# Kernel tuning notes

Measured on AMD Instinct MI355X. Metric: run time of the kernel, lower is better.

## Reference

```python
import jax, jax.numpy as jnp
import numpy as np

B, S, D, H, FF = 2, 2048, 1024, 16, 4096
DK = D // H
LOCAL_WINDOW, STRIDE = 128, 128
NEG = -1000000000.0
EPS = 1e-5


def _layernorm(x, g, b):
    mu = jnp.mean(x, axis=-1, keepdims=True)
    var = jnp.mean(jnp.square(x - mu), axis=-1, keepdims=True)
    return (x - mu) * jax.lax.rsqrt(var + EPS) * g + b


def _strided_mask(seq):
    # allowed(i, j): j <= i and (i-j <= local_window or (i-j) % stride == 0)
    i = jnp.arange(seq)[:, None]
    j = jnp.arange(seq)[None, :]
    d = i - j
    return (d >= 0) & ((d <= LOCAL_WINDOW) | (d % STRIDE == 0))  # [S, S] bool


def setup_inputs() -> dict:
    key = jax.random.key(0)
    ks = jax.random.split(key, 18)
    w = lambda k, shape: jax.random.normal(k, shape, jnp.float32) * 0.02
    return {
        "x": jax.random.normal(ks[0], (B, S, D), jnp.float32),
        "mask": jnp.ones((1, 1, S, S), jnp.int32),
        "Wq": w(ks[1], (D, D)), "bq": jnp.zeros((D,), jnp.float32),
        "Wk": w(ks[2], (D, D)), "bk": jnp.zeros((D,), jnp.float32),
        "Wv": w(ks[3], (D, D)), "bv": jnp.zeros((D,), jnp.float32),
        "Wo": w(ks[4], (D, D)), "bo": jnp.zeros((D,), jnp.float32),
        "W1": w(ks[5], (D, FF)), "bf1": jnp.zeros((FF,), jnp.float32),
        "W2": w(ks[6], (FF, D)), "bf2": jnp.zeros((D,), jnp.float32),
        "g1": jnp.ones((D,), jnp.float32), "bl1": jnp.zeros((D,), jnp.float32),
        "g2": jnp.ones((D,), jnp.float32), "bl2": jnp.zeros((D,), jnp.float32),
    }


def reference(x, mask, Wq, bq, Wk, bk, Wv, bv, Wo, bo,
              W1, bf1, W2, bf2, g1, bl1, g2, bl2):
    b, s, d = x.shape
    sm = _strided_mask(s)[None, None]  # [1,1,S,S]

    # pre-LN self-attention
    n = _layernorm(x, g1, bl1)
    split = lambda t: t.reshape(b, s, H, DK).transpose(0, 2, 1, 3)  # [B,H,S,DK]
    q = split(n @ Wq + bq)
    k = split(n @ Wk + bk)
    v = split(n @ Wv + bv)

    scores = jnp.einsum('bhqd,bhkd->bhqk', q, k) / jnp.sqrt(jnp.float32(DK))
    scores = jnp.where(sm, scores, NEG)          # strided/local mask
    scores = jnp.where(mask == 0, NEG, scores)   # user mask
    attn = jax.nn.softmax(scores, axis=-1)
    o = jnp.einsum('bhqk,bhkd->bhqd', attn, v)
    o = o.transpose(0, 2, 1, 3).reshape(b, s, d) @ Wo + bo
    x = x + o

    # pre-LN FFN (GELU exact, matching torch nn.GELU default)
    n2 = _layernorm(x, g2, bl2)
    ff = jax.nn.gelu(n2 @ W1 + bf1, approximate=False) @ W2 + bf2
    return x + ff
```

## Files before the change

kernel.cpp:

```cpp
#include <hip/hip_runtime.h>
#include <math.h>

typedef unsigned int u32;
typedef unsigned short u16;

#define B_  2
#define S_  2048
#define D_  1024
#define H_  16
#define DK_ 64
#define FF_ 4096
#define NEG_ -1000000000.0f

typedef __attribute__((ext_vector_type(8))) short short8;
typedef __attribute__((ext_vector_type(4))) float floatx4;
typedef __attribute__((ext_vector_type(4))) unsigned short ushort4_t;

__device__ inline u16 f2b(float f) {
    union { float f; u32 u; } v; v.f = f;
    u32 r = (v.u + 0x7fffu + ((v.u >> 16) & 1u)) >> 16;
    return (u16)r;
}
__device__ inline float b2f(u16 b) {
    union { u32 u; float f; } v; v.u = ((u32)b) << 16;
    return v.f;
}

__device__ inline void gl_lds16(const u16* g, u16* l) {
    __builtin_amdgcn_global_load_lds((const __attribute__((address_space(1))) u32*)g,
                                     (__attribute__((address_space(3))) u32*)l, 16, 0, 0);
}

__global__ void tconv4(const float* __restrict__ W0, const float* __restrict__ W1_,
                       const float* __restrict__ W2_, const float* __restrict__ W3,
                       u16* __restrict__ dstBase) {
    __shared__ float tile[32][33];
    int z = blockIdx.z;
    const float* Wm = (z == 0) ? W0 : (z == 1) ? W1_ : (z == 2) ? W2_ : W3;
    u16* Wt = dstBase + (size_t)z * 1024 * 1024;
    const int K = 1024, N = 1024;
    int n0 = blockIdx.x * 32, k0 = blockIdx.y * 32;
    int tx = threadIdx.x & 31, ty = threadIdx.x >> 5;
#pragma unroll
    for (int r = 0; r < 32; r += 8)
        tile[ty + r][tx] = Wm[(size_t)(k0 + ty + r) * N + n0 + tx];
    __syncthreads();
#pragma unroll
    for (int r = 0; r < 32; r += 8)
        Wt[(size_t)(n0 + ty + r) * K + k0 + tx] = f2b(tile[tx][ty + r]);
}

__global__ void tconv(const float* __restrict__ Wm, u16* __restrict__ Wt, int K, int N) {
    __shared__ float tile[32][33];
    int n0 = blockIdx.x * 32, k0 = blockIdx.y * 32;
    int tx = threadIdx.x & 31, ty = threadIdx.x >> 5;
#pragma unroll
    for (int r = 0; r < 32; r += 8)
        tile[ty + r][tx] = Wm[(size_t)(k0 + ty + r) * N + n0 + tx];
    __syncthreads();
#pragma unroll
    for (int r = 0; r < 32; r += 8)
        Wt[(size_t)(n0 + ty + r) * K + k0 + tx] = f2b(tile[tx][ty + r]);
}

__global__ void catbias(const float* __restrict__ bq, const float* __restrict__ bk,
                        const float* __restrict__ bv, float* __restrict__ out) {
    int i = blockIdx.x * 256 + threadIdx.x;
    float v = (i < 1024) ? bq[i] : (i < 2048) ? bk[i - 1024] : bv[i - 2048];
    out[i] = v;
}

__global__ void ln_bf16(const float* __restrict__ x, const float* __restrict__ g,
                        const float* __restrict__ b, u16* __restrict__ out) {
    int row = blockIdx.x;
    int t = threadIdx.x;
    const float* xr = x + (size_t)row * D_;
    __shared__ float red[256];

    float s = 0.f;
    for (int i = t; i < D_; i += 256) s += xr[i];
    red[t] = s; __syncthreads();
    for (int off = 128; off > 0; off >>= 1) {
        if (t < off) red[t] += red[t + off];
        __syncthreads();
    }
    float mu = red[0] * (1.0f / D_);
    __syncthreads();

    float vs = 0.f;
    for (int i = t; i < D_; i += 256) { float d = xr[i] - mu; vs += d * d; }
    red[t] = vs; __syncthreads();
    for (int off = 128; off > 0; off >>= 1) {
        if (t < off) red[t] += red[t + off];
        __syncthreads();
    }
    float rstd = rsqrtf(red[0] * (1.0f / D_) + 1e-5f);

    u16* outr = out + (size_t)row * D_;
    for (int i = t; i < D_; i += 256)
        outr[i] = f2b((xr[i] - mu) * rstd * g[i] + b[i]);
}

template <int EPI>
__global__ __launch_bounds__(256)
void gemm_bt(const u16* __restrict__ A, const u16* __restrict__ Bt,
             const float* __restrict__ bias, const float* __restrict__ R,
             void* __restrict__ Cv, int M, int N, int K, int ldA, int ldB) {
    __shared__ u16 As[2 * 128 * 32];
    __shared__ u16 Bs[2 * 128 * 32];
    int tid = threadIdx.x;
    int lane = tid & 63, w = tid >> 6;
    int wm = w >> 1, wn = w & 1;
    int m0 = blockIdx.x * 128, n0 = blockIdx.y * 128;
    size_t koff = (size_t)blockIdx.z * K;

    floatx4 acc[4][4];
#pragma unroll
    for (int a = 0; a < 4; a++)
#pragma unroll
        for (int b2 = 0; b2 < 4; b2++) acc[a][b2] = (floatx4){0.f, 0.f, 0.f, 0.f};

    int r4 = lane >> 2;
    int qg = ((lane & 3) ^ ((lane >> 3) & 3)) * 8;
    const u16* Ag0 = A + (size_t)(m0 + w * 16 + r4) * ldA + koff + qg;
    const u16* Bg0 = Bt + (size_t)(n0 + w * 16 + r4) * ldB + koff + qg;
    u16* Al = As + (w * 16) * 32;
    u16* Bl = Bs + (w * 16) * 32;

    int c = lane & 15, g = lane >> 4;
    int sw = (g ^ ((c >> 1) & 3)) * 8;
    const u16* pa[4];
    const u16* pb[4];
#pragma unroll
    for (int a = 0; a < 4; a++) pa[a] = &As[(wm * 64 + a * 16 + c) * 32 + sw];
#pragma unroll
    for (int b2 = 0; b2 < 4; b2++) pb[b2] = &Bs[(wn * 64 + b2 * 16 + c) * 32 + sw];

    for (int k0 = 0; k0 < K; k0 += 64) {
        __syncthreads();
        gl_lds16(Ag0 + k0,                      Al);
        gl_lds16(Ag0 + k0 + (size_t)64 * ldA,   Al + 64 * 32);
        gl_lds16(Ag0 + k0 + 32,                 Al + 128 * 32);
        gl_lds16(Ag0 + k0 + 32 + (size_t)64 * ldA, Al + 192 * 32);
        gl_lds16(Bg0 + k0,                      Bl);
        gl_lds16(Bg0 + k0 + (size_t)64 * ldB,   Bl + 64 * 32);
        gl_lds16(Bg0 + k0 + 32,                 Bl + 128 * 32);
        gl_lds16(Bg0 + k0 + 32 + (size_t)64 * ldB, Bl + 192 * 32);
        __syncthreads();

        short8 fa[4], fb[4];
#pragma unroll
        for (int a = 0; a < 4; a++) fa[a] = *(const short8*)pa[a];
#pragma unroll
        for (int b2 = 0; b2 < 4; b2++) fb[b2] = *(const short8*)pb[b2];
#pragma unroll
        for (int a = 0; a < 4; a++)
#pragma unroll
            for (int b2 = 0; b2 < 4; b2++)
                acc[a][b2] = __builtin_amdgcn_mfma_f32_16x16x32_bf16(fa[a], fb[b2], acc[a][b2], 0, 0, 0);
#pragma unroll
        for (int a = 0; a < 4; a++) fa[a] = *(const short8*)(pa[a] + 128 * 32);
#pragma unroll
        for (int b2 = 0; b2 < 4; b2++) fb[b2] = *(const short8*)(pb[b2] + 128 * 32);
#pragma unroll
        for (int a = 0; a < 4; a++)
#pragma unroll
            for (int b2 = 0; b2 < 4; b2++)
                acc[a][b2] = __builtin_amdgcn_mfma_f32_16x16x32_bf16(fa[a], fb[b2], acc[a][b2], 0, 0, 0);
    }

    int mb = m0 + wm * 64, nb = n0 + wn * 64;
#pragma unroll
    for (int a = 0; a < 4; a++) {
#pragma unroll
        for (int b2 = 0; b2 < 4; b2++) {
            int mrow = mb + a * 16 + (lane >> 4) * 4;
            int ncol = nb + b2 * 16 + (lane & 15);
            float bv = (EPI == 3) ? 0.f : bias[ncol];
#pragma unroll
            for (int r = 0; r < 4; r++) {
                int m = mrow + r;
                float vvv = acc[a][b2][r] + bv;
                if (EPI == 0) {
                    int which = ncol >> 10, col = ncol & 1023;
                    int bb = m >> 11, ss = m & 2047, hh = col >> 6, dk = col & 63;
                    ((u16*)Cv)[(size_t)which * ((size_t)B_ * S_ * D_) +
                               ((((size_t)bb * H_ + hh) * S_) + ss) * DK_ + dk] = f2b(vvv);
                } else if (EPI == 1) {
                    ((float*)Cv)[(size_t)m * N + ncol] = vvv + R[(size_t)m * N + ncol];
                } else if (EPI == 2) {
                    ((u16*)Cv)[(size_t)m * N + ncol] =
                        f2b(0.5f * vvv * (1.f + erff(vvv * 0.70710678118654752f)));
                } else {
                    ((u16*)Cv)[(size_t)blockIdx.z * M * N + (size_t)m * N + ncol] = f2b(vvv);
                }
            }
        }
    }
}

__global__ __launch_bounds__(256)
void ffn2_merge(const u16* __restrict__ P, const float* __restrict__ x1,
                const float* __restrict__ bf2, float* __restrict__ out) {
    const size_t MN = (size_t)B_ * S_ * D_;
    int e = (blockIdx.x * 256 + threadIdx.x) * 4;
    float4 xv = *(const float4*)&x1[e];
    float4 bv = *(const float4*)&bf2[e & 1023];
    float o0 = xv.x + bv.x, o1 = xv.y + bv.y, o2 = xv.z + bv.z, o3 = xv.w + bv.w;
#pragma unroll
    for (int z = 0; z < 4; z++) {
        ushort4_t pv = *(const ushort4_t*)&P[z * MN + e];
        o0 += b2f(pv[0]); o1 += b2f(pv[1]); o2 += b2f(pv[2]); o3 += b2f(pv[3]);
    }
    *(float4*)&out[e] = (float4){o0, o1, o2, o3};
}

__global__ __launch_bounds__(256)
void attn3(const u16* __restrict__ q, const u16* __restrict__ k,
           const u16* __restrict__ v, const int* __restrict__ mask,
           u16* __restrict__ ob) {
    __shared__ u16 Qs[64 * 72];
    __shared__ u16 Kw[192 * 72];
    __shared__ u16 Vt[64 * 200];
    __shared__ u16 Vband[4][16 * 64];
    __shared__ float sb[64][17];

    const int i0 = blockIdx.x * 64;
    const int bh = blockIdx.y;
    const int b  = bh >> 4, h = bh & 15;
    const int t  = threadIdx.x;
    const int lane = t & 63, w = t >> 6;
    const int c = lane & 15, g = lane >> 4;
    const int qloc16 = w * 16;

    const u16* qg = q + ((size_t)bh * S_ + i0) * DK_;
    const u16* kg = k + (size_t)bh * S_ * DK_;
    const u16* vg = v + (size_t)bh * S_ * DK_;

    const int wlo = (i0 >= 128) ? i0 - 128 : 0;
    const int wn  = i0 + 64 - wlo;
    const int nb  = (i0 >= 256) ? (i0 >> 7) - 1 : 0;
    const int jb0 = i0 & 127;
    const int dd0 = i0 - wlo;

    for (int e = t; e < 64 * 8; e += 256) {
        int row = e >> 3, dc = e & 7;
        *(short8*)&Qs[row * 72 + dc * 8] = *(const short8*)(qg + row * 64 + dc * 8);
    }
    for (int e = t; e < wn * 8; e += 256) {
        int row = e >> 3, dc = e & 7;
        *(short8*)&Kw[row * 72 + dc * 8] = *(const short8*)(kg + (size_t)(wlo + row) * 64 + dc * 8);
    }
#pragma unroll
    for (int dc = 0; dc < 8; dc++) {
        for (int jl = t; jl < 192; jl += 256) {
            short8 val = {0, 0, 0, 0, 0, 0, 0, 0};
            if (jl < wn) val = *(const short8*)(vg + (size_t)(wlo + jl) * 64 + dc * 8);
#pragma unroll
            for (int i = 0; i < 8; i++) Vt[(dc * 8 + i) * 200 + jl] = (u16)val[i];
        }
    }
    __syncthreads();

    for (int m = 0; m < nb; m++) {
        int jb = jb0 + (m << 7);
        int jrow = jb + qloc16 + c;
        float p = 0.f;
#pragma unroll
        for (int kc = 0; kc < 2; kc++) {
            short8 kv = *(const short8*)(kg + (size_t)jrow * 64 + kc * 32 + g * 8);
            short8 qv = *(const short8*)&Qs[(qloc16 + c) * 72 + kc * 32 + g * 8];
#pragma unroll
            for (int i = 0; i < 8; i++) p += b2f((u16)qv[i]) * b2f((u16)kv[i]);
        }
        p += __shfl_xor(p, 16);
        p += __shfl_xor(p, 32);
        if (g == 0) {
            int qi = i0 + qloc16 + c;
            float s = p * 0.125f;
            if (mask[(size_t)qi * S_ + jrow] == 0) s = NEG_;
            sb[qloc16 + c][m] = s;
        }
    }

    floatx4 sc[12];
#pragma unroll
    for (int ct = 0; ct < 12; ct++) sc[ct] = (floatx4){0.f, 0.f, 0.f, 0.f};
    short8 fa0 = *(const short8*)&Qs[(qloc16 + c) * 72 + g * 8];
    short8 fa1 = *(const short8*)&Qs[(qloc16 + c) * 72 + 32 + g * 8];
#pragma unroll
    for (int ct = 0; ct < 12; ct++) {
        short8 fb0 = *(const short8*)&Kw[(ct * 16 + c) * 72 + g * 8];
        short8 fb1 = *(const short8*)&Kw[(ct * 16 + c) * 72 + 32 + g * 8];
        sc[ct] = __builtin_amdgcn_mfma_f32_16x16x32_bf16(fa0, fb0, sc[ct], 0, 0, 0);
        sc[ct] = __builtin_amdgcn_mfma_f32_16x16x32_bf16(fa1, fb1, sc[ct], 0, 0, 0);
    }

#pragma unroll
    for (int ct = 0; ct < 12; ct++) {
        int cidx = ct * 16 + c;
        int j = wlo + cidx;
#pragma unroll
        for (int r = 0; r < 4; r++) {
            int qloc = qloc16 + g * 4 + r;
            int d = dd0 + qloc - cidx;
            float s = sc[ct][r] * 0.125f;
            bool ok = false;
            if (d >= 0 && d <= 128) ok = (mask[(size_t)(i0 + qloc) * S_ + j] != 0);
            sc[ct][r] = ok ? s : NEG_;
        }
    }

    float mv[4], inv[4];
#pragma unroll
    for (int r = 0; r < 4; r++) {
        float mm = -1e30f;
#pragma unroll
        for (int ct = 0; ct < 12; ct++) mm = fmaxf(mm, sc[ct][r]);
        mm = fmaxf(mm, __shfl_xor(mm, 1));
        mm = fmaxf(mm, __shfl_xor(mm, 2));
        mm = fmaxf(mm, __shfl_xor(mm, 4));
        mm = fmaxf(mm, __shfl_xor(mm, 8));
        int qloc = qloc16 + g * 4 + r;
        for (int m = 0; m < nb; m++) mm = fmaxf(mm, sb[qloc][m]);
        float sum = 0.f;
#pragma unroll
        for (int ct = 0; ct < 12; ct++) {
            float e = __expf(sc[ct][r] - mm);
            sc[ct][r] = e;
            sum += e;
        }
        sum += __shfl_xor(sum, 1);
        sum += __shfl_xor(sum, 2);
        sum += __shfl_xor(sum, 4);
        sum += __shfl_xor(sum, 8);
        for (int m = 0; m < nb; m++) sum += __expf(sb[qloc][m] - mm);
        mv[r] = mm;
        inv[r] = 1.f / sum;
    }

    __syncthreads();
    u16* P = Kw;
#pragma unroll
    for (int ct = 0; ct < 12; ct++) {
#pragma unroll
        for (int r = 0; r < 4; r++) {
            int qloc = qloc16 + g * 4 + r;
            P[qloc * 200 + ct * 16 + c] = f2b(sc[ct][r]);
        }
    }

    floatx4 o[4];
#pragma unroll
    for (int nt = 0; nt < 4; nt++) o[nt] = (floatx4){0.f, 0.f, 0.f, 0.f};
#pragma unroll
    for (int ks = 0; ks < 6; ks++) {
        short8 pa = *(const short8*)&P[(qloc16 + c) * 200 + ks * 32 + g * 8];
#pragma unroll
        for (int nt = 0; nt < 4; nt++) {
            short8 vb = *(const short8*)&Vt[(nt * 16 + c) * 200 + ks * 32 + g * 8];
            o[nt] = __builtin_amdgcn_mfma_f32_16x16x32_bf16(pa, vb, o[nt], 0, 0, 0);
        }
    }

    for (int m = 0; m < nb; m++) {
        int jb = jb0 + (m << 7);
        asm volatile("s_waitcnt lgkmcnt(0)" ::: "memory");
        __builtin_amdgcn_wave_barrier();
        gl_lds16(vg + (size_t)(jb + qloc16 + (lane >> 3)) * 64 + (lane & 7) * 8, &Vband[w][0]);
        gl_lds16(vg + (size_t)(jb + qloc16 + 8 + (lane >> 3)) * 64 + (lane & 7) * 8, &Vband[w][512]);
        asm volatile("s_waitcnt vmcnt(0)" ::: "memory");
        __builtin_amdgcn_wave_barrier();
#pragma unroll
        for (int r = 0; r < 4; r++) {
            int qloc = qloc16 + g * 4 + r;
            float pb = __expf(sb[qloc][m] - mv[r]);
#pragma unroll
            for (int nt = 0; nt < 4; nt++)
                o[nt][r] += pb * b2f(Vband[w][(g * 4 + r) * 64 + nt * 16 + c]);
        }
    }

#pragma unroll
    for (int nt = 0; nt < 4; nt++) {
#pragma unroll
        for (int r = 0; r < 4; r++) {
            int qi = i0 + qloc16 + g * 4 + r;
            ob[((size_t)b * S_ + qi) * D_ + h * 64 + nt * 16 + c] = f2b(o[nt][r] * inv[r]);
        }
    }
}

extern "C" void kernel_launch(void* const* d_in, const int* in_sizes, int n_in,
                              void* d_out, int out_size, void* d_ws, size_t ws_size,
                              hipStream_t stream) {
    const float* x    = (const float*)d_in[0];
    const int*   mask = (const int*)  d_in[1];
    const float* Wq   = (const float*)d_in[2];
    const float* bq   = (const float*)d_in[3];
    const float* Wk   = (const float*)d_in[4];
    const float* bk   = (const float*)d_in[5];
    const float* Wv   = (const float*)d_in[6];
    const float* bv   = (const float*)d_in[7];
    const float* Wo   = (const float*)d_in[8];
    const float* bo   = (const float*)d_in[9];
    const float* W1   = (const float*)d_in[10];
    const float* bf1  = (const float*)d_in[11];
    const float* W2   = (const float*)d_in[12];
    const float* bf2  = (const float*)d_in[13];
    const float* g1   = (const float*)d_in[14];
    const float* bl1  = (const float*)d_in[15];
    const float* g2   = (const float*)d_in[16];
    const float* bl2  = (const float*)d_in[17];

    char* wsb = (char*)d_ws;
    const size_t MB = 1024 * 1024;
    u16*   WtQKV = (u16*)(wsb + 0);
    u16*   WtO   = (u16*)(wsb + 6 * MB);
    u16*   Wt1   = (u16*)(wsb + 8 * MB);
    u16*   Wt2   = (u16*)(wsb + 16 * MB);
    u16*   n1b   = (u16*)(wsb + 24 * MB);
    u16*   qkv   = (u16*)(wsb + 32 * MB);
    u16*   obb   = (u16*)(wsb + 56 * MB);
    float* x1    = (float*)(wsb + 32 * MB);
    u16*   ff1b  = (u16*)(wsb + 48 * MB);
    u16*   Ppart = (u16*)(wsb + 82 * MB);
    float* bcat  = (float*)(wsb + 114 * MB);
    u16*   n2b   = n1b;

    const int M = B_ * S_;
    const size_t SZ = (size_t)B_ * S_ * D_;

    tconv4<<<dim3(32, 32, 4), 256, 0, stream>>>(Wq, Wk, Wv, Wo, WtQKV);
    tconv<<<dim3(128, 32), 256, 0, stream>>>(W1, Wt1, 1024, 4096);
    tconv<<<dim3(32, 128), 256, 0, stream>>>(W2, Wt2, 4096, 1024);
    catbias<<<12, 256, 0, stream>>>(bq, bk, bv, bcat);

    ln_bf16<<<M, 256, 0, stream>>>(x, g1, bl1, n1b);

    gemm_bt<0><<<dim3(32, 24), 256, 0, stream>>>(n1b, WtQKV, bcat, nullptr, qkv,
                                                 M, 3072, 1024, 1024, 1024);

    attn3<<<dim3(32, 32), 256, 0, stream>>>(qkv, qkv + SZ, qkv + 2 * SZ, mask, obb);

    gemm_bt<1><<<dim3(32, 8), 256, 0, stream>>>(obb, WtO, bo, x, x1,
                                                M, 1024, 1024, 1024, 1024);

    ln_bf16<<<M, 256, 0, stream>>>(x1, g2, bl2, n2b);

    gemm_bt<2><<<dim3(32, 32), 256, 0, stream>>>(n2b, Wt1, bf1, nullptr, ff1b,
                                                 M, 4096, 1024, 1024, 1024);

    gemm_bt<3><<<dim3(32, 8, 4), 256, 0, stream>>>(ff1b, Wt2, nullptr, nullptr, Ppart,
                                                   M, 1024, 1024, 4096, 4096);
    ffn2_merge<<<(int)(SZ / 1024), 256, 0, stream>>>(Ppart, x1, bf2, (float*)d_out);
}
```

Before: 447.3 us.

## Double-buffer GEMM loads, split-K out-projection with fused merge+LayerNorm, tanh GELU

```diff
diff --git a/kernel.cpp b/kernel.cpp
--- a/kernel.cpp
+++ b/kernel.cpp
@@ -77,8 +77,10 @@
     const float* xr = x + (size_t)row * D_;
     __shared__ float red[256];
 
+    float v[4];
     float s = 0.f;
-    for (int i = t; i < D_; i += 256) s += xr[i];
+#pragma unroll
+    for (int i = 0; i < 4; i++) { v[i] = xr[i * 256 + t]; s += v[i]; }
     red[t] = s; __syncthreads();
     for (int off = 128; off > 0; off >>= 1) {
         if (t < off) red[t] += red[t + off];
@@ -88,7 +90,8 @@
     __syncthreads();
 
     float vs = 0.f;
-    for (int i = t; i < D_; i += 256) { float d = xr[i] - mu; vs += d * d; }
+#pragma unroll
+    for (int i = 0; i < 4; i++) { float d = v[i] - mu; vs += d * d; }
     red[t] = vs; __syncthreads();
     for (int off = 128; off > 0; off >>= 1) {
         if (t < off) red[t] += red[t + off];
@@ -97,17 +100,64 @@
     float rstd = rsqrtf(red[0] * (1.0f / D_) + 1e-5f);
 
     u16* outr = out + (size_t)row * D_;
-    for (int i = t; i < D_; i += 256)
-        outr[i] = f2b((xr[i] - mu) * rstd * g[i] + b[i]);
+#pragma unroll
+    for (int i = 0; i < 4; i++) {
+        int col = i * 256 + t;
+        outr[col] = f2b((v[i] - mu) * rstd * g[col] + b[col]);
+    }
+}
+
+__global__ __launch_bounds__(256)
+void merge_ln(const u16* __restrict__ P, const float* __restrict__ x,
+              const float* __restrict__ bo, const float* __restrict__ g,
+              const float* __restrict__ bl, float* __restrict__ x1,
+              u16* __restrict__ n2) {
+    const size_t MN = (size_t)B_ * S_ * D_;
+    int row = blockIdx.x, t = threadIdx.x;
+    size_t base = (size_t)row * D_;
+    __shared__ float red[256];
+
+    float v[4];
+    float s = 0.f;
+#pragma unroll
+    for (int i = 0; i < 4; i++) {
+        int col = i * 256 + t;
+        float val = x[base + col] + bo[col] + b2f(P[base + col]) + b2f(P[MN + base + col]);
+        v[i] = val; s += val;
+    }
+    red[t] = s; __syncthreads();
+    for (int off = 128; off > 0; off >>= 1) {
+        if (t < off) red[t] += red[t + off];
+        __syncthreads();
+    }
+    float mu = red[0] * (1.0f / D_);
+    __syncthreads();
+
+    float vs = 0.f;
+#pragma unroll
+    for (int i = 0; i < 4; i++) { float d = v[i] - mu; vs += d * d; }
+    red[t] = vs; __syncthreads();
+    for (int off = 128; off > 0; off >>= 1) {
+        if (t < off) red[t] += red[t + off];
+        __syncthreads();
+    }
+    float rstd = rsqrtf(red[0] * (1.0f / D_) + 1e-5f);
+
+#pragma unroll
+    for (int i = 0; i < 4; i++) {
+        int col = i * 256 + t;
+        x1[base + col] = v[i];
+        n2[base + col] = f2b((v[i] - mu) * rstd * g[col] + bl[col]);
+    }
 }
 
 template <int EPI>
-__global__ __launch_bounds__(256)
+__global__ __launch_bounds__(256, 4)
 void gemm_bt(const u16* __restrict__ A, const u16* __restrict__ Bt,
              const float* __restrict__ bias, const float* __restrict__ R,
              void* __restrict__ Cv, int M, int N, int K, int ldA, int ldB) {
-    __shared__ u16 As[2 * 128 * 32];
-    __shared__ u16 Bs[2 * 128 * 32];
+    __shared__ u16 As[2][128 * 32];
+    __shared__ u16 Bs[2][128 * 32];
     int tid = threadIdx.x;
     int lane = tid & 63, w = tid >> 6;
     int wm = w >> 1, wn = w & 1;
@@ -124,49 +174,40 @@
     int qg = ((lane & 3) ^ ((lane >> 3) & 3)) * 8;
     const u16* Ag0 = A + (size_t)(m0 + w * 16 + r4) * ldA + koff + qg;
     const u16* Bg0 = Bt + (size_t)(n0 + w * 16 + r4) * ldB + koff + qg;
-    u16* Al = As + (w * 16) * 32;
-    u16* Bl = Bs + (w * 16) * 32;
+    const int ldsOff = (w * 16) * 32;
 
     int c = lane & 15, g = lane >> 4;
     int sw = (g ^ ((c >> 1) & 3)) * 8;
-    const u16* pa[4];
-    const u16* pb[4];
-#pragma unroll
-    for (int a = 0; a < 4; a++) pa[a] = &As[(wm * 64 + a * 16 + c) * 32 + sw];
-#pragma unroll
-    for (int b2 = 0; b2 < 4; b2++) pb[b2] = &Bs[(wn * 64 + b2 * 16 + c) * 32 + sw];
-
-    for (int k0 = 0; k0 < K; k0 += 64) {
+
+    const int nIter = K >> 5;
+
+    gl_lds16(Ag0, &As[0][ldsOff]);
+    gl_lds16(Ag0 + (size_t)64 * ldA, &As[0][ldsOff + 64 * 32]);
+    gl_lds16(Bg0, &Bs[0][ldsOff]);
+    gl_lds16(Bg0 + (size_t)64 * ldB, &Bs[0][ldsOff + 64 * 32]);
+
+    for (int it = 0; it < nIter; it++) {
         __syncthreads();
-        gl_lds16(Ag0 + k0,                      Al);
-        gl_lds16(Ag0 + k0 + (size_t)64 * ldA,   Al + 64 * 32);
-        gl_lds16(Ag0 + k0 + 32,                 Al + 128 * 32);
-        gl_lds16(Ag0 + k0 + 32 + (size_t)64 * ldA, Al + 192 * 32);
-        gl_lds16(Bg0 + k0,                      Bl);
-        gl_lds16(Bg0 + k0 + (size_t)64 * ldB,   Bl + 64 * 32);
-        gl_lds16(Bg0 + k0 + 32,                 Bl + 128 * 32);
-        gl_lds16(Bg0 + k0 + 32 + (size_t)64 * ldB, Bl + 192 * 32);
-        __syncthreads();
-
+        int cur = it & 1, nxt = cur ^ 1;
+        if (it + 1 < nIter) {
+            int kk = (it + 1) << 5;
+            gl_lds16(Ag0 + kk, &As[nxt][ldsOff]);
+            gl_lds16(Ag0 + kk + (size_t)64 * ldA, &As[nxt][ldsOff + 64 * 32]);
+            gl_lds16(Bg0 + kk, &Bs[nxt][ldsOff]);
+            gl_lds16(Bg0 + kk + (size_t)64 * ldB, &Bs[nxt][ldsOff + 64 * 32]);
+        }
         short8 fa[4], fb[4];
 #pragma unroll
-        for (int a = 0; a < 4; a++) fa[a] = *(const short8*)pa[a];
-#pragma unroll
-        for (int b2 = 0; b2 < 4; b2++) fb[b2] = *(const short8*)pb[b2];
+        for (int a = 0; a < 4; a++)
+            fa[a] = *(const short8*)&As[cur][(wm * 64 + a * 16 + c) * 32 + sw];
+#pragma unroll
+        for (int b2 = 0; b2 < 4; b2++)
+            fb[b2] = *(const short8*)&Bs[cur][(wn * 64 + b2 * 16 + c) * 32 + sw];
 #pragma unroll
         for (int a = 0; a < 4; a++)
 #pragma unroll
             for (int b2 = 0; b2 < 4; b2++)
                 acc[a][b2] = __builtin_amdgcn_mfma_f32_16x16x32_bf16(fa[a], fb[b2], acc[a][b2], 0, 0, 0);
-#pragma unroll
-        for (int a = 0; a < 4; a++) fa[a] = *(const short8*)(pa[a] + 128 * 32);
-#pragma unroll
-        for (int b2 = 0; b2 < 4; b2++) fb[b2] = *(const short8*)(pb[b2] + 128 * 32);
-#pragma unroll
-        for (int a = 0; a < 4; a++)
-#pragma unroll
-            for (int b2 = 0; b2 < 4; b2++)
-                acc[a][b2] = __builtin_amdgcn_mfma_f32_16x16x32_bf16(fa[a], fb[b2], acc[a][b2], 0, 0, 0);
     }
 
     int mb = m0 + wm * 64, nb = n0 + wn * 64;
@@ -174,8 +215,8 @@
     for (int a = 0; a < 4; a++) {
 #pragma unroll
         for (int b2 = 0; b2 < 4; b2++) {
-            int mrow = mb + a * 16 + (lane >> 4) * 4;
-            int ncol = nb + b2 * 16 + (lane & 15);
+            int mrow = mb + a * 16 + g * 4;
+            int ncol = nb + b2 * 16 + c;
             float bv = (EPI == 3) ? 0.f : bias[ncol];
 #pragma unroll
             for (int r = 0; r < 4; r++) {
@@ -189,8 +230,9 @@
                 } else if (EPI == 1) {
                     ((float*)Cv)[(size_t)m * N + ncol] = vvv + R[(size_t)m * N + ncol];
                 } else if (EPI == 2) {
-                    ((u16*)Cv)[(size_t)m * N + ncol] =
-                        f2b(0.5f * vvv * (1.f + erff(vvv * 0.70710678118654752f)));
+                    float u = 0.79788456080286536f * fmaf(0.044715f * vvv, vvv * vvv, vvv);
+                    float th = 1.f - 2.f / (1.f + __expf(2.f * u));
+                    ((u16*)Cv)[(size_t)m * N + ncol] = f2b(0.5f * vvv * (1.f + th));
                 } else {
                     ((u16*)Cv)[(size_t)blockIdx.z * M * N + (size_t)m * N + ncol] = f2b(vvv);
                 }
@@ -415,18 +457,19 @@
 
     char* wsb = (char*)d_ws;
     const size_t MB = 1024 * 1024;
-    u16*   WtQKV = (u16*)(wsb + 0);
-    u16*   WtO   = (u16*)(wsb + 6 * MB);
-    u16*   Wt1   = (u16*)(wsb + 8 * MB);
-    u16*   Wt2   = (u16*)(wsb + 16 * MB);
-    u16*   n1b   = (u16*)(wsb + 24 * MB);
-    u16*   qkv   = (u16*)(wsb + 32 * MB);
-    u16*   obb   = (u16*)(wsb + 56 * MB);
-    float* x1    = (float*)(wsb + 32 * MB);
-    u16*   ff1b  = (u16*)(wsb + 48 * MB);
-    u16*   Ppart = (u16*)(wsb + 82 * MB);
-    float* bcat  = (float*)(wsb + 114 * MB);
-    u16*   n2b   = n1b;
+    u16*   WtQKV  = (u16*)(wsb + 0);
+    u16*   WtO    = (u16*)(wsb + 6 * MB);
+    u16*   Wt1    = (u16*)(wsb + 8 * MB);
+    u16*   Wt2    = (u16*)(wsb + 16 * MB);
+    u16*   n1b    = (u16*)(wsb + 24 * MB);
+    u16*   qkv    = (u16*)(wsb + 32 * MB);
+    u16*   obb    = (u16*)(wsb + 56 * MB);
+    float* x1     = (float*)(wsb + 32 * MB);
+    u16*   ff1b   = (u16*)(wsb + 48 * MB);
+    u16*   Ppart  = (u16*)(wsb + 82 * MB);
+    u16*   PpartO = (u16*)(wsb + 82 * MB);
+    float* bcat   = (float*)(wsb + 114 * MB);
+    u16*   n2b    = n1b;
 
     const int M = B_ * S_;
     const size_t SZ = (size_t)B_ * S_ * D_;
@@ -443,10 +486,9 @@
 
     attn3<<<dim3(32, 32), 256, 0, stream>>>(qkv, qkv + SZ, qkv + 2 * SZ, mask, obb);
 
-    gemm_bt<1><<<dim3(32, 8), 256, 0, stream>>>(obb, WtO, bo, x, x1,
-                                                M, 1024, 1024, 1024, 1024);
-
-    ln_bf16<<<M, 256, 0, stream>>>(x1, g2, bl2, n2b);
+    gemm_bt<3><<<dim3(32, 8, 2), 256, 0, stream>>>(obb, WtO, nullptr, nullptr, PpartO,
+                                                   M, 1024, 512, 1024, 1024);
+    merge_ln<<<M, 256, 0, stream>>>(PpartO, x, bo, g2, bl2, x1, n2b);
 
     gemm_bt<2><<<dim3(32, 32), 256, 0, stream>>>(n2b, Wt1, bf1, nullptr, ff1b,
                                                  M, 4096, 1024, 1024, 1024);
```

Result: faster. 404.7 us (-9.5%).
